# Optimization experiments

Measured on AMD Instinct MI355X. Metric: run time of the kernel, lower is better.

Reference implementation:

```python
import jax, jax.numpy as jnp
import numpy as np

EPS = 1e-5

def _layernorm(x, gamma, beta):
    # LayerNormalization over last axis (channels), epsilon=1e-5
    mu = jnp.mean(x, axis=-1, keepdims=True)
    var = jnp.var(x, axis=-1, keepdims=True)
    return (x - mu) * jax.lax.rsqrt(var + EPS) * gamma + beta

def setup_inputs() -> dict:
    key = jax.random.key(0)
    ks = jax.random.split(key, 6)
    B, H, W, C = 8, 64, 64, 256
    std = 0.1  # NIN init_scale
    return {
        "x": jax.random.normal(ks[0], (B, H, W, C), dtype=jnp.float32),
        "ln_gamma": jnp.ones((C,), dtype=jnp.float32),
        "ln_beta": jnp.zeros((C,), dtype=jnp.float32),
        "wq": jax.random.normal(ks[1], (C, C), dtype=jnp.float32) * std,
        "bq": jnp.zeros((C,), dtype=jnp.float32),
        "wk": jax.random.normal(ks[2], (C, C), dtype=jnp.float32) * std,
        "bk": jnp.zeros((C,), dtype=jnp.float32),
        "wv": jax.random.normal(ks[3], (C, C), dtype=jnp.float32) * std,
        "bv": jnp.zeros((C,), dtype=jnp.float32),
        "wo": jax.random.normal(ks[4], (C, C), dtype=jnp.float32) * std,
        "bo": jnp.zeros((C,), dtype=jnp.float32),
    }

def reference(x, ln_gamma, ln_beta, wq, bq, wk, bk, wv, bv, wo, bo):
    B, H, W, C = x.shape
    h = _layernorm(x, ln_gamma, ln_beta)
    # 1x1 convs == per-pixel channel matmuls
    q = jnp.einsum('bhwc,cd->bhwd', h, wq) + bq
    k = jnp.einsum('bhwc,cd->bhwd', h, wk) + bk
    v = jnp.einsum('bhwc,cd->bhwd', h, wv) + bv
    scale = jnp.float32(C) ** -0.5
    # dense spatial attention over all H*W tokens
    w = jnp.einsum('bhwc,bijc->bhwij', q, k) * scale  # [B,H,W,H,W]
    w = jax.nn.softmax(w.reshape(B, H, W, H * W), axis=-1).reshape(B, H, W, H, W)
    h = jnp.einsum('bhwij,bijc->bhwc', w, v)
    h = jnp.einsum('bhwc,cd->bhwd', h, wo) + bo
    return x + h
```

## Files before the change

kernel.cpp:

```cpp
#include <hip/hip_runtime.h>
#include <stdint.h>

#define NB    8
#define NTOK  4096
#define TOK   32768
#define CDIM  256
#define BQ    128
#define BK    64
#define NT    (NTOK / BK)

#define KPITCH 264
#define VPITCH 68
#define KTILE_SH (BK * KPITCH)
#define VTILE_SH (CDIM * VPITCH)
#define KCH   33
#define VCH   34
#define TOTCH (KCH + VCH)

typedef __attribute__((ext_vector_type(8))) short bf16x8;
typedef __attribute__((ext_vector_type(4))) float f32x4;

#define SSCALE 0.09016844f

static __device__ __forceinline__ unsigned short f2bf(float f) {
    union { float f; unsigned u; } v; v.f = f;
    unsigned r = v.u + 0x7fffu + ((v.u >> 16) & 1u);
    return (unsigned short)(r >> 16);
}

static __device__ __forceinline__ void dma16(const unsigned short* g, unsigned short* l) {
    __builtin_amdgcn_global_load_lds(
        (const __attribute__((address_space(1))) unsigned int*)g,
        (__attribute__((address_space(3))) unsigned int*)l,
        16, 0, 0);
}

__global__ __launch_bounds__(256) void prep_kernel(
        const float* __restrict__ x,
        const float* __restrict__ gamma,
        const float* __restrict__ beta,
        const float* __restrict__ w0, const float* __restrict__ w1,
        const float* __restrict__ w2, const float* __restrict__ w3,
        unsigned short* __restrict__ h_bf,
        unsigned short* __restrict__ wt) {
    int bx = blockIdx.x;
    if (bx >= TOK / 4) {
        int id = bx - TOK / 4;
        int m = id >> 8, dd = id & 255;
        const float* src = (m == 0) ? w0 : (m == 1) ? w1 : (m == 2) ? w2 : w3;
        wt[m * (CDIM * CDIM) + dd * CDIM + threadIdx.x] = f2bf(src[threadIdx.x * CDIM + dd]);
        return;
    }
    int w = threadIdx.x >> 6;
    int lane = threadIdx.x & 63;
    int token = bx * 4 + w;
    const float4 xv = ((const float4*)(x + (size_t)token * CDIM))[lane];
    float s = xv.x + xv.y + xv.z + xv.w;
    #pragma unroll
    for (int off = 1; off < 64; off <<= 1) s += __shfl_xor(s, off, 64);
    float mean = s * (1.0f / 256.0f);
    float d0 = xv.x - mean, d1 = xv.y - mean, d2 = xv.z - mean, d3 = xv.w - mean;
    float ss = d0 * d0 + d1 * d1 + d2 * d2 + d3 * d3;
    #pragma unroll
    for (int off = 1; off < 64; off <<= 1) ss += __shfl_xor(ss, off, 64);
    float rstd = rsqrtf(ss * (1.0f / 256.0f) + 1e-5f);
    float4 g = ((const float4*)gamma)[lane];
    float4 b = ((const float4*)beta)[lane];
    ushort4 o;
    o.x = f2bf(d0 * rstd * g.x + b.x);
    o.y = f2bf(d1 * rstd * g.y + b.y);
    o.z = f2bf(d2 * rstd * g.z + b.z);
    o.w = f2bf(d3 * rstd * g.w + b.w);
    ((ushort4*)(h_bf + (size_t)token * CDIM))[lane] = o;
}

__global__ __launch_bounds__(128) void qk_kernel(
        const unsigned short* __restrict__ h_bf,
        const unsigned short* __restrict__ wts,
        const float* __restrict__ bq,
        const float* __restrict__ bk,
        unsigned short* __restrict__ q_bf,
        unsigned short* __restrict__ k2) {
    int by = blockIdx.y;
    const unsigned short* wt = wts + (size_t)by * (CDIM * CDIM);
    const float* bias = (by == 0) ? bq : bk;
    float oscale = (by == 0) ? SSCALE : 1.0f;
    int w = threadIdx.x >> 6, lane = threadIdx.x & 63;
    int quad = lane >> 4, l16 = lane & 15;
    int tok_base = blockIdx.x * 64 + w * 32;

    bf16x8 afr[2][8];
    #pragma unroll
    for (int s = 0; s < 2; ++s)
        #pragma unroll
        for (int kk = 0; kk < 8; ++kk)
            afr[s][kk] = *(const bf16x8*)(h_bf + (size_t)(tok_base + s * 16 + l16) * CDIM + kk * 32 + quad * 8);

    unsigned short* kdst = k2 + (size_t)blockIdx.x * KTILE_SH;

    #pragma unroll
    for (int nt = 0; nt < 16; ++nt) {
        f32x4 acc0 = {0.f, 0.f, 0.f, 0.f};
        f32x4 acc1 = {0.f, 0.f, 0.f, 0.f};
        #pragma unroll
        for (int kk = 0; kk < 8; ++kk) {
            bf16x8 bfr = *(const bf16x8*)(wt + (size_t)(nt * 16 + l16) * CDIM + kk * 32 + quad * 8);
            acc0 = __builtin_amdgcn_mfma_f32_16x16x32_bf16(afr[0][kk], bfr, acc0, 0, 0, 0);
            acc1 = __builtin_amdgcn_mfma_f32_16x16x32_bf16(afr[1][kk], bfr, acc1, 0, 0, 0);
        }
        int d = nt * 16 + l16;
        float bb = bias[d];
        if (by == 0) {
            #pragma unroll
            for (int r = 0; r < 4; ++r) {
                q_bf[(size_t)(tok_base + quad * 4 + r) * CDIM + d]      = f2bf((acc0[r] + bb) * oscale);
                q_bf[(size_t)(tok_base + 16 + quad * 4 + r) * CDIM + d] = f2bf((acc1[r] + bb) * oscale);
            }
        } else {
            int row0 = w * 32 + quad * 4;
            #pragma unroll
            for (int r = 0; r < 4; ++r) {
                kdst[(size_t)(row0 + r) * KPITCH + d]      = f2bf(acc0[r] + bb);
                kdst[(size_t)(row0 + 16 + r) * KPITCH + d] = f2bf(acc1[r] + bb);
            }
        }
    }
}

__global__ __launch_bounds__(128) void vproj_kernel(
        const unsigned short* __restrict__ h_bf,
        const unsigned short* __restrict__ wv_t,
        const float* __restrict__ bv,
        unsigned short* __restrict__ vt2) {
    __shared__ unsigned short VT[CDIM][VPITCH];
    int tid = threadIdx.x;
    int w = tid >> 6, lane = tid & 63, quad = lane >> 4, l16 = lane & 15;
    int tok_base = blockIdx.x * 64 + w * 32;

    bf16x8 afr[2][8];
    #pragma unroll
    for (int s = 0; s < 2; ++s)
        #pragma unroll
        for (int kk = 0; kk < 8; ++kk)
            afr[s][kk] = *(const bf16x8*)(h_bf + (size_t)(tok_base + s * 16 + l16) * CDIM + kk * 32 + quad * 8);

    #pragma unroll
    for (int nt = 0; nt < 16; ++nt) {
        f32x4 acc0 = {0.f, 0.f, 0.f, 0.f};
        f32x4 acc1 = {0.f, 0.f, 0.f, 0.f};
        #pragma unroll
        for (int kk = 0; kk < 8; ++kk) {
            bf16x8 bfr = *(const bf16x8*)(wv_t + (size_t)(nt * 16 + l16) * CDIM + kk * 32 + quad * 8);
            acc0 = __builtin_amdgcn_mfma_f32_16x16x32_bf16(afr[0][kk], bfr, acc0, 0, 0, 0);
            acc1 = __builtin_amdgcn_mfma_f32_16x16x32_bf16(afr[1][kk], bfr, acc1, 0, 0, 0);
        }
        int d = nt * 16 + l16;
        float bb = bv[d];
        int col0 = w * 32 + quad * 4;
        #pragma unroll
        for (int r = 0; r < 4; ++r) {
            VT[d][col0 + r]      = f2bf(acc0[r] + bb);
            VT[d][col0 + 16 + r] = f2bf(acc1[r] + bb);
        }
    }
    __syncthreads();
    const uint4* src = (const uint4*)(&VT[0][0]);
    uint4* dst = (uint4*)(vt2 + (size_t)blockIdx.x * VTILE_SH);
    #pragma unroll
    for (int i = 0; i < 17; ++i)
        dst[i * 128 + tid] = src[i * 128 + tid];
}

#define DMA_TILE(KS, VS, ktn)                                                        \
    {                                                                                \
        const unsigned short* gk = k2 + (size_t)(b * NT + (ktn)) * KTILE_SH;         \
        const unsigned short* gv = vt2 + (size_t)(b * NT + (ktn)) * VTILE_SH;        \
        for (int c = w; c < TOTCH; c += 8) {                                         \
            if (c < KCH) dma16(gk + c * 512 + lane * 8, &KS[0][0] + c * 512);        \
            else dma16(gv + (c - KCH) * 512 + lane * 8, &VS[0][0] + (c - KCH) * 512);\
        }                                                                            \
    }

#define COMPUTE_TILE(KS, VS)                                                         \
    {                                                                                \
        f32x4 sfr[2][2];                                                             \
        _Pragma("unroll")                                                            \
        for (int nt = 0; nt < 2; ++nt) {                                             \
            f32x4 a0 = {0.f, 0.f, 0.f, 0.f};                                         \
            f32x4 a1 = {0.f, 0.f, 0.f, 0.f};                                         \
            _Pragma("unroll")                                                        \
            for (int kk = 0; kk < 8; ++kk) {                                         \
                bf16x8 kb = *(const bf16x8*)(&KS[kh * 32 + nt * 16 + l16][kk * 32 + quad * 8]); \
                a0 = __builtin_amdgcn_mfma_f32_16x16x32_bf16(qfr[0][kk], kb, a0, 0, 0, 0);      \
                a1 = __builtin_amdgcn_mfma_f32_16x16x32_bf16(qfr[1][kk], kb, a1, 0, 0, 0);      \
            }                                                                        \
            sfr[0][nt] = a0; sfr[1][nt] = a1;                                        \
        }                                                                            \
        _Pragma("unroll")                                                            \
        for (int s = 0; s < 2; ++s)                                                  \
            _Pragma("unroll")                                                        \
            for (int nt = 0; nt < 2; ++nt)                                           \
                _Pragma("unroll")                                                    \
                for (int r = 0; r < 4; ++r) {                                        \
                    float p = exp2f(sfr[s][nt][r]);                                  \
                    lacc[s][r] += p;                                                 \
                    Pl[wq * 32 + s * 16 + quad * 4 + r][kh * 32 + nt * 16 + l16] =   \
                        (unsigned short)(__float_as_uint(p) >> 16);                  \
                }                                                                    \
        bf16x8 pfr0 = *(const bf16x8*)(&Pl[wq * 32 + l16][kh * 32 + quad * 8]);      \
        bf16x8 pfr1 = *(const bf16x8*)(&Pl[wq * 32 + 16 + l16][kh * 32 + quad * 8]); \
        _Pragma("unroll")                                                            \
        for (int nt2 = 0; nt2 < 16; ++nt2) {                                         \
            bf16x8 vb = *(const bf16x8*)(&VS[nt2 * 16 + l16][kh * 32 + quad * 8]);   \
            O[0][nt2] = __builtin_amdgcn_mfma_f32_16x16x32_bf16(pfr0, vb, O[0][nt2], 0, 0, 0);  \
            O[1][nt2] = __builtin_amdgcn_mfma_f32_16x16x32_bf16(pfr1, vb, O[1][nt2], 0, 0, 0);  \
        }                                                                            \
    }

__global__ __launch_bounds__(512, 2) void flash_kernel(
        const unsigned short* __restrict__ q_bf,
        const unsigned short* __restrict__ k2,
        const unsigned short* __restrict__ vt2,
        unsigned short* __restrict__ attn) {
    __shared__ unsigned short Ks0[BK][KPITCH];
    __shared__ unsigned short Ks1[BK][KPITCH];
    __shared__ unsigned short Vs0[CDIM][VPITCH];
    __shared__ unsigned short Vs1[CDIM][VPITCH];
    __shared__ unsigned short Pl[BQ][VPITCH];

    int tid = threadIdx.x;
    int w = tid >> 6, lane = tid & 63, quad = lane >> 4, l16 = lane & 15;
    int kh = w >> 2;
    int wq = w & 3;
    int bid = blockIdx.x;
    int b = bid & 7;
    int qtile = bid >> 3;
    int qrow = qtile * BQ + wq * 32;
    const size_t bbase = (size_t)b * NTOK * CDIM;

    bf16x8 qfr[2][8];
    #pragma unroll
    for (int s = 0; s < 2; ++s)
        #pragma unroll
        for (int kk = 0; kk < 8; ++kk)
            qfr[s][kk] = *(const bf16x8*)(q_bf + bbase + (size_t)(qrow + s * 16 + l16) * CDIM + kk * 32 + quad * 8);

    f32x4 O[2][16];
    #pragma unroll
    for (int s = 0; s < 2; ++s)
        #pragma unroll
        for (int i = 0; i < 16; ++i) O[s][i] = (f32x4){0.f, 0.f, 0.f, 0.f};
    float lacc[2][4] = {{0.f, 0.f, 0.f, 0.f}, {0.f, 0.f, 0.f, 0.f}};

    DMA_TILE(Ks0, Vs0, 0);
    __syncthreads();

    for (int kt2 = 0; kt2 < NT; kt2 += 2) {
        DMA_TILE(Ks1, Vs1, kt2 + 1);
        COMPUTE_TILE(Ks0, Vs0);
        __syncthreads();
        if (kt2 + 2 < NT) DMA_TILE(Ks0, Vs0, kt2 + 2);
        COMPUTE_TILE(Ks1, Vs1);
        __syncthreads();
    }

    float* sO = (wq == 0) ? (float*)&Ks0[0][0] : (wq == 1) ? (float*)&Ks1[0][0]
              : (wq == 2) ? (float*)&Vs0[0][0] : (float*)&Vs1[0][0];
    float* sL = (float*)&Pl[0][0] + wq * 512;

    if (kh == 1) {
        #pragma unroll
        for (int s = 0; s < 2; ++s) {
            #pragma unroll
            for (int nt2 = 0; nt2 < 16; ++nt2)
                #pragma unroll
                for (int r = 0; r < 4; ++r)
                    sO[((s * 16 + nt2) * 4 + r) * 64 + lane] = O[s][nt2][r];
            #pragma unroll
            for (int r = 0; r < 4; ++r)
                sL[(s * 4 + r) * 64 + lane] = lacc[s][r];
        }
    }
    __syncthreads();
    if (kh == 0) {
        float linv[2][4];
        #pragma unroll
        for (int s = 0; s < 2; ++s)
            #pragma unroll
            for (int r = 0; r < 4; ++r) {
                float ls = lacc[s][r] + sL[(s * 4 + r) * 64 + lane];
                #pragma unroll
                for (int off = 1; off < 16; off <<= 1)
                    ls += __shfl_xor(ls, off, 64);
                linv[s][r] = 1.0f / ls;
            }
        #pragma unroll
        for (int s = 0; s < 2; ++s)
            #pragma unroll
            for (int nt2 = 0; nt2 < 16; ++nt2) {
                int d = nt2 * 16 + l16;
                #pragma unroll
                for (int r = 0; r < 4; ++r) {
                    float val = (O[s][nt2][r] + sO[((s * 16 + nt2) * 4 + r) * 64 + lane]) * linv[s][r];
                    attn[bbase + (size_t)(qrow + s * 16 + quad * 4 + r) * CDIM + d] = f2bf(val);
                }
            }
    }
}

__global__ __launch_bounds__(128) void oproj_kernel(
        const unsigned short* __restrict__ attn,
        const unsigned short* __restrict__ wo_t,
        const float* __restrict__ bo,
        const float* __restrict__ x,
        float* __restrict__ out) {
    int w = threadIdx.x >> 6, lane = threadIdx.x & 63;
    int quad = lane >> 4, l16 = lane & 15;
    int tok_base = blockIdx.x * 64 + w * 32;

    bf16x8 afr[2][8];
    #pragma unroll
    for (int s = 0; s < 2; ++s)
        #pragma unroll
        for (int kk = 0; kk < 8; ++kk)
            afr[s][kk] = *(const bf16x8*)(attn + (size_t)(tok_base + s * 16 + l16) * CDIM + kk * 32 + quad * 8);

    #pragma unroll
    for (int nt = 0; nt < 16; ++nt) {
        f32x4 acc0 = {0.f, 0.f, 0.f, 0.f};
        f32x4 acc1 = {0.f, 0.f, 0.f, 0.f};
        #pragma unroll
        for (int kk = 0; kk < 8; ++kk) {
            bf16x8 bfr = *(const bf16x8*)(wo_t + (size_t)(nt * 16 + l16) * CDIM + kk * 32 + quad * 8);
            acc0 = __builtin_amdgcn_mfma_f32_16x16x32_bf16(afr[0][kk], bfr, acc0, 0, 0, 0);
            acc1 = __builtin_amdgcn_mfma_f32_16x16x32_bf16(afr[1][kk], bfr, acc1, 0, 0, 0);
        }
        int d = nt * 16 + l16;
        float bb = bo[d];
        #pragma unroll
        for (int r = 0; r < 4; ++r) {
            size_t idx0 = (size_t)(tok_base + quad * 4 + r) * CDIM + d;
            size_t idx1 = (size_t)(tok_base + 16 + quad * 4 + r) * CDIM + d;
            out[idx0] = x[idx0] + acc0[r] + bb;
            out[idx1] = x[idx1] + acc1[r] + bb;
        }
    }
}

extern "C" void kernel_launch(void* const* d_in, const int* in_sizes, int n_in,
                              void* d_out, int out_size, void* d_ws, size_t ws_size,
                              hipStream_t stream) {
    const float* x     = (const float*)d_in[0];
    const float* gamma = (const float*)d_in[1];
    const float* beta  = (const float*)d_in[2];
    const float* wq    = (const float*)d_in[3];
    const float* bq    = (const float*)d_in[4];
    const float* wk    = (const float*)d_in[5];
    const float* bk    = (const float*)d_in[6];
    const float* wv    = (const float*)d_in[7];
    const float* bv    = (const float*)d_in[8];
    const float* wo    = (const float*)d_in[9];
    const float* bo    = (const float*)d_in[10];
    float* out = (float*)d_out;

    char* ws = (char*)d_ws;
    unsigned short* h_bf = (unsigned short*)(ws);
    unsigned short* q_bf = (unsigned short*)(ws + 16777216);
    unsigned short* k2   = (unsigned short*)(ws + 33554432);
    unsigned short* vt2  = (unsigned short*)(ws + 50855936);
    unsigned short* wt   = (unsigned short*)(ws + 68681728);
    unsigned short* attn = h_bf;

    prep_kernel<<<TOK / 4 + 1024, 256, 0, stream>>>(x, gamma, beta, wq, wk, wv, wo, h_bf, wt);
    qk_kernel<<<dim3(TOK / 64, 2), 128, 0, stream>>>(h_bf, wt, bq, bk, q_bf, k2);
    vproj_kernel<<<TOK / 64, 128, 0, stream>>>(h_bf, wt + 2 * (CDIM * CDIM), bv, vt2);
    flash_kernel<<<(NTOK / BQ) * NB, 512, 0, stream>>>(q_bf, k2, vt2, attn);
    oproj_kernel<<<TOK / 64, 128, 0, stream>>>(attn, wt + 3 * (CDIM * CDIM), bo, x, out);
}
```

Measured before the change: 379.4 us.

## Fuse Q/K/V projections into one kernel and precompute flash LDS offsets

After: 713.2 us. 1.88x slower.

```diff
diff --git a/kernel.cpp b/kernel.cpp
--- a/kernel.cpp
+++ b/kernel.cpp
@@ -74,115 +74,109 @@
     ((ushort4*)(h_bf + (size_t)token * CDIM))[lane] = o;
 }
 
-__global__ __launch_bounds__(128) void qk_kernel(
+__global__ __launch_bounds__(256) void qkv_kernel(
         const unsigned short* __restrict__ h_bf,
         const unsigned short* __restrict__ wts,
         const float* __restrict__ bq,
         const float* __restrict__ bk,
+        const float* __restrict__ bv,
         unsigned short* __restrict__ q_bf,
-        unsigned short* __restrict__ k2) {
-    int by = blockIdx.y;
-    const unsigned short* wt = wts + (size_t)by * (CDIM * CDIM);
-    const float* bias = (by == 0) ? bq : bk;
-    float oscale = (by == 0) ? SSCALE : 1.0f;
-    int w = threadIdx.x >> 6, lane = threadIdx.x & 63;
-    int quad = lane >> 4, l16 = lane & 15;
-    int tok_base = blockIdx.x * 64 + w * 32;
-
-    bf16x8 afr[2][8];
-    #pragma unroll
-    for (int s = 0; s < 2; ++s)
-        #pragma unroll
-        for (int kk = 0; kk < 8; ++kk)
-            afr[s][kk] = *(const bf16x8*)(h_bf + (size_t)(tok_base + s * 16 + l16) * CDIM + kk * 32 + quad * 8);
-
-    unsigned short* kdst = k2 + (size_t)blockIdx.x * KTILE_SH;
-
-    #pragma unroll
-    for (int nt = 0; nt < 16; ++nt) {
-        f32x4 acc0 = {0.f, 0.f, 0.f, 0.f};
-        f32x4 acc1 = {0.f, 0.f, 0.f, 0.f};
-        #pragma unroll
-        for (int kk = 0; kk < 8; ++kk) {
-            bf16x8 bfr = *(const bf16x8*)(wt + (size_t)(nt * 16 + l16) * CDIM + kk * 32 + quad * 8);
-            acc0 = __builtin_amdgcn_mfma_f32_16x16x32_bf16(afr[0][kk], bfr, acc0, 0, 0, 0);
-            acc1 = __builtin_amdgcn_mfma_f32_16x16x32_bf16(afr[1][kk], bfr, acc1, 0, 0, 0);
-        }
-        int d = nt * 16 + l16;
-        float bb = bias[d];
-        if (by == 0) {
-            #pragma unroll
-            for (int r = 0; r < 4; ++r) {
-                q_bf[(size_t)(tok_base + quad * 4 + r) * CDIM + d]      = f2bf((acc0[r] + bb) * oscale);
-                q_bf[(size_t)(tok_base + 16 + quad * 4 + r) * CDIM + d] = f2bf((acc1[r] + bb) * oscale);
-            }
-        } else {
-            int row0 = w * 32 + quad * 4;
-            #pragma unroll
-            for (int r = 0; r < 4; ++r) {
-                kdst[(size_t)(row0 + r) * KPITCH + d]      = f2bf(acc0[r] + bb);
-                kdst[(size_t)(row0 + 16 + r) * KPITCH + d] = f2bf(acc1[r] + bb);
-            }
-        }
-    }
-}
-
-__global__ __launch_bounds__(128) void vproj_kernel(
-        const unsigned short* __restrict__ h_bf,
-        const unsigned short* __restrict__ wv_t,
-        const float* __restrict__ bv,
+        unsigned short* __restrict__ k2,
         unsigned short* __restrict__ vt2) {
     __shared__ unsigned short VT[CDIM][VPITCH];
     int tid = threadIdx.x;
     int w = tid >> 6, lane = tid & 63, quad = lane >> 4, l16 = lane & 15;
-    int tok_base = blockIdx.x * 64 + w * 32;
-
-    bf16x8 afr[2][8];
-    #pragma unroll
-    for (int s = 0; s < 2; ++s)
-        #pragma unroll
-        for (int kk = 0; kk < 8; ++kk)
-            afr[s][kk] = *(const bf16x8*)(h_bf + (size_t)(tok_base + s * 16 + l16) * CDIM + kk * 32 + quad * 8);
-
-    #pragma unroll
-    for (int nt = 0; nt < 16; ++nt) {
-        f32x4 acc0 = {0.f, 0.f, 0.f, 0.f};
-        f32x4 acc1 = {0.f, 0.f, 0.f, 0.f};
-        #pragma unroll
-        for (int kk = 0; kk < 8; ++kk) {
-            bf16x8 bfr = *(const bf16x8*)(wv_t + (size_t)(nt * 16 + l16) * CDIM + kk * 32 + quad * 8);
-            acc0 = __builtin_amdgcn_mfma_f32_16x16x32_bf16(afr[0][kk], bfr, acc0, 0, 0, 0);
-            acc1 = __builtin_amdgcn_mfma_f32_16x16x32_bf16(afr[1][kk], bfr, acc1, 0, 0, 0);
-        }
-        int d = nt * 16 + l16;
-        float bb = bv[d];
-        int col0 = w * 32 + quad * 4;
-        #pragma unroll
-        for (int r = 0; r < 4; ++r) {
-            VT[d][col0 + r]      = f2bf(acc0[r] + bb);
-            VT[d][col0 + 16 + r] = f2bf(acc1[r] + bb);
+    int blk = blockIdx.x;
+    int tok_base = blk * 64 + w * 16;
+
+    bf16x8 afr[8];
+    #pragma unroll
+    for (int kk = 0; kk < 8; ++kk)
+        afr[kk] = *(const bf16x8*)(h_bf + (size_t)(tok_base + l16) * CDIM + kk * 32 + quad * 8);
+
+    {
+        const unsigned short* wq_t = wts;
+        #pragma unroll
+        for (int nt = 0; nt < 16; ++nt) {
+            f32x4 acc = {0.f, 0.f, 0.f, 0.f};
+            #pragma unroll
+            for (int kk = 0; kk < 8; ++kk) {
+                bf16x8 bfr = *(const bf16x8*)(wq_t + (size_t)(nt * 16 + l16) * CDIM + kk * 32 + quad * 8);
+                acc = __builtin_amdgcn_mfma_f32_16x16x32_bf16(afr[kk], bfr, acc, 0, 0, 0);
+            }
+            int d = nt * 16 + l16;
+            float bb = bq[d];
+            #pragma unroll
+            for (int r = 0; r < 4; ++r)
+                q_bf[(size_t)(tok_base + quad * 4 + r) * CDIM + d] = f2bf((acc[r] + bb) * SSCALE);
+        }
+    }
+    {
+        const unsigned short* wk_t = wts + CDIM * CDIM;
+        unsigned short* kdst = k2 + (size_t)blk * KTILE_SH;
+        int row0 = w * 16 + quad * 4;
+        #pragma unroll
+        for (int nt = 0; nt < 16; ++nt) {
+            f32x4 acc = {0.f, 0.f, 0.f, 0.f};
+            #pragma unroll
+            for (int kk = 0; kk < 8; ++kk) {
+                bf16x8 bfr = *(const bf16x8*)(wk_t + (size_t)(nt * 16 + l16) * CDIM + kk * 32 + quad * 8);
+                acc = __builtin_amdgcn_mfma_f32_16x16x32_bf16(afr[kk], bfr, acc, 0, 0, 0);
+            }
+            int d = nt * 16 + l16;
+            float bb = bk[d];
+            #pragma unroll
+            for (int r = 0; r < 4; ++r)
+                kdst[(size_t)(row0 + r) * KPITCH + d] = f2bf(acc[r] + bb);
+        }
+    }
+    {
+        const unsigned short* wv_t = wts + 2 * CDIM * CDIM;
+        int col0 = w * 16 + quad * 4;
+        #pragma unroll
+        for (int nt = 0; nt < 16; ++nt) {
+            f32x4 acc = {0.f, 0.f, 0.f, 0.f};
+            #pragma unroll
+            for (int kk = 0; kk < 8; ++kk) {
+                bf16x8 bfr = *(const bf16x8*)(wv_t + (size_t)(nt * 16 + l16) * CDIM + kk * 32 + quad * 8);
+                acc = __builtin_amdgcn_mfma_f32_16x16x32_bf16(afr[kk], bfr, acc, 0, 0, 0);
+            }
+            int d = nt * 16 + l16;
+            float bb = bv[d];
+            #pragma unroll
+            for (int r = 0; r < 4; ++r)
+                VT[d][col0 + r] = f2bf(acc[r] + bb);
         }
     }
     __syncthreads();
     const uint4* src = (const uint4*)(&VT[0][0]);
-    uint4* dst = (uint4*)(vt2 + (size_t)blockIdx.x * VTILE_SH);
-    #pragma unroll
-    for (int i = 0; i < 17; ++i)
-        dst[i * 128 + tid] = src[i * 128 + tid];
-}
-
-#define DMA_TILE(KS, VS, ktn)                                                        \
+    uint4* dst = (uint4*)(vt2 + (size_t)blk * VTILE_SH);
+    #pragma unroll
+    for (int i = 0; i < 9; ++i) {
+        int idx = i * 256 + tid;
+        if (idx < (VTILE_SH / 8)) dst[idx] = src[idx];
+    }
+}
+
+#define DMA_TILE(KS, VS)                                                             \
     {                                                                                \
-        const unsigned short* gk = k2 + (size_t)(b * NT + (ktn)) * KTILE_SH;         \
-        const unsigned short* gv = vt2 + (size_t)(b * NT + (ktn)) * VTILE_SH;        \
-        for (int c = w; c < TOTCH; c += 8) {                                         \
+        _Pragma("unroll")                                                            \
+        for (int i = 0; i < 8; ++i) {                                                \
+            int c = w + i * 8;                                                       \
             if (c < KCH) dma16(gk + c * 512 + lane * 8, &KS[0][0] + c * 512);        \
             else dma16(gv + (c - KCH) * 512 + lane * 8, &VS[0][0] + (c - KCH) * 512);\
         }                                                                            \
+        if (w < 3) {                                                                 \
+            int c = 64 + w;                                                          \
+            dma16(gv + (c - KCH) * 512 + lane * 8, &VS[0][0] + (c - KCH) * 512);     \
+        }                                                                            \
+        gk += KTILE_SH; gv += VTILE_SH;                                              \
     }
 
 #define COMPUTE_TILE(KS, VS)                                                         \
     {                                                                                \
+        const unsigned short* KsF = &KS[0][0] + kbase;                               \
+        const unsigned short* VsF = &VS[0][0] + vbase;                               \
         f32x4 sfr[2][2];                                                             \
         _Pragma("unroll")                                                            \
         for (int nt = 0; nt < 2; ++nt) {                                             \
@@ -190,7 +184,7 @@
             f32x4 a1 = {0.f, 0.f, 0.f, 0.f};                                         \
             _Pragma("unroll")                                                        \
             for (int kk = 0; kk < 8; ++kk) {                                         \
-                bf16x8 kb = *(const bf16x8*)(&KS[kh * 32 + nt * 16 + l16][kk * 32 + quad * 8]); \
+                bf16x8 kb = *(const bf16x8*)(KsF + nt * 16 * KPITCH + kk * 32);      \
                 a0 = __builtin_amdgcn_mfma_f32_16x16x32_bf16(qfr[0][kk], kb, a0, 0, 0, 0);      \
                 a1 = __builtin_amdgcn_mfma_f32_16x16x32_bf16(qfr[1][kk], kb, a1, 0, 0, 0);      \
             }                                                                        \
@@ -204,14 +198,14 @@
                 for (int r = 0; r < 4; ++r) {                                        \
                     float p = exp2f(sfr[s][nt][r]);                                  \
                     lacc[s][r] += p;                                                 \
-                    Pl[wq * 32 + s * 16 + quad * 4 + r][kh * 32 + nt * 16 + l16] =   \
+                    pw[(s * 16 + r) * VPITCH + nt * 16] =                            \
                         (unsigned short)(__float_as_uint(p) >> 16);                  \
                 }                                                                    \
-        bf16x8 pfr0 = *(const bf16x8*)(&Pl[wq * 32 + l16][kh * 32 + quad * 8]);      \
-        bf16x8 pfr1 = *(const bf16x8*)(&Pl[wq * 32 + 16 + l16][kh * 32 + quad * 8]); \
+        bf16x8 pfr0 = *(const bf16x8*)(pr);                                          \
+        bf16x8 pfr1 = *(const bf16x8*)(pr + 16 * VPITCH);                            \
         _Pragma("unroll")                                                            \
         for (int nt2 = 0; nt2 < 16; ++nt2) {                                         \
-            bf16x8 vb = *(const bf16x8*)(&VS[nt2 * 16 + l16][kh * 32 + quad * 8]);   \
+            bf16x8 vb = *(const bf16x8*)(VsF + nt2 * 16 * VPITCH);                   \
             O[0][nt2] = __builtin_amdgcn_mfma_f32_16x16x32_bf16(pfr0, vb, O[0][nt2], 0, 0, 0);  \
             O[1][nt2] = __builtin_amdgcn_mfma_f32_16x16x32_bf16(pfr1, vb, O[1][nt2], 0, 0, 0);  \
         }                                                                            \
@@ -238,6 +232,14 @@
     int qrow = qtile * BQ + wq * 32;
     const size_t bbase = (size_t)b * NTOK * CDIM;
 
+    const int kbase = (kh * 32 + l16) * KPITCH + quad * 8;
+    const int vbase = l16 * VPITCH + kh * 32 + quad * 8;
+    unsigned short* pw = &Pl[0][0] + (wq * 32 + quad * 4) * VPITCH + kh * 32 + l16;
+    const unsigned short* pr = &Pl[0][0] + (wq * 32 + l16) * VPITCH + kh * 32 + quad * 8;
+
+    const unsigned short* gk = k2 + (size_t)b * NT * KTILE_SH;
+    const unsigned short* gv = vt2 + (size_t)b * NT * VTILE_SH;
+
     bf16x8 qfr[2][8];
     #pragma unroll
     for (int s = 0; s < 2; ++s)
@@ -252,14 +254,14 @@
         for (int i = 0; i < 16; ++i) O[s][i] = (f32x4){0.f, 0.f, 0.f, 0.f};
     float lacc[2][4] = {{0.f, 0.f, 0.f, 0.f}, {0.f, 0.f, 0.f, 0.f}};
 
-    DMA_TILE(Ks0, Vs0, 0);
+    DMA_TILE(Ks0, Vs0);
     __syncthreads();
 
     for (int kt2 = 0; kt2 < NT; kt2 += 2) {
-        DMA_TILE(Ks1, Vs1, kt2 + 1);
+        DMA_TILE(Ks1, Vs1);
         COMPUTE_TILE(Ks0, Vs0);
         __syncthreads();
-        if (kt2 + 2 < NT) DMA_TILE(Ks0, Vs0, kt2 + 2);
+        if (kt2 + 2 < NT) DMA_TILE(Ks0, Vs0);
         COMPUTE_TILE(Ks1, Vs1);
         __syncthreads();
     }
@@ -372,8 +374,7 @@
     unsigned short* attn = h_bf;
 
     prep_kernel<<<TOK / 4 + 1024, 256, 0, stream>>>(x, gamma, beta, wq, wk, wv, wo, h_bf, wt);
-    qk_kernel<<<dim3(TOK / 64, 2), 128, 0, stream>>>(h_bf, wt, bq, bk, q_bf, k2);
-    vproj_kernel<<<TOK / 64, 128, 0, stream>>>(h_bf, wt + 2 * (CDIM * CDIM), bv, vt2);
+    qkv_kernel<<<TOK / 64, 256, 0, stream>>>(h_bf, wt, bq, bk, bv, q_bf, k2, vt2);
     flash_kernel<<<(NTOK / BQ) * NB, 512, 0, stream>>>(q_bf, k2, vt2, attn);
     oproj_kernel<<<TOK / 64, 128, 0, stream>>>(attn, wt + 3 * (CDIM * CDIM), bo, x, out);
 }
```
